# Optimization experiments

Hardware: AMD Instinct MI355X
Metric: run time of the kernel (lower is better)

The kernel has to match this reference:

```python
import jax, jax.numpy as jnp
import numpy as np

EPS = 1e-8


def setup_inputs() -> dict:
    key = jax.random.key(0)
    k1, k2, k3, k4, k5 = jax.random.split(key, 5)
    B, N_LOG, N_PHYS, E = 16, 512, 2048, 2048
    P = jax.random.uniform(k1, (B, N_LOG, N_PHYS), dtype=jnp.float32)
    d_hw = jax.random.randint(k2, (N_PHYS, N_PHYS), 0, 4, dtype=jnp.int32)
    edge_src = jax.random.randint(k3, (B, E), 0, N_LOG, dtype=jnp.int32)
    edge_dst = jax.random.randint(k4, (B, E), 0, N_LOG, dtype=jnp.int32)
    edge_w = jax.random.uniform(k5, (B, E), dtype=jnp.float32)
    return {"P": P, "d_hw": d_hw, "edge_src": edge_src,
            "edge_dst": edge_dst, "edge_w": edge_w}


def reference(P, d_hw, edge_src, edge_dst, edge_w):
    # A_hw[p,q] = 1 where hardware distance == 1 (adjacent qubits)
    A_hw = (d_hw == 1).astype(P.dtype)                      # [Q, Q]
    B = P.shape[0]
    # Dense contraction once per batch: PA[b,i,q] = sum_p P[b,i,p] A[p,q]
    PA = jnp.einsum('bip,pq->biq', P, A_hw)                 # [B, N, Q]
    b_idx = jnp.arange(B)[:, None]                          # [B, 1]
    gi = PA[b_idx, edge_src]                                # [B, E, Q]
    gj = P[b_idx, edge_dst]                                 # [B, E, Q]
    adj_score = jnp.einsum('beq,beq->be', gi, gj)           # [B, E]
    sample_adj = jnp.sum(edge_w * adj_score, axis=-1)       # [B]
    sample_weight = jnp.maximum(jnp.sum(edge_w, axis=-1), EPS)
    # every sample has edges -> valid_samples = B
    loss = -jnp.mean(sample_adj / sample_weight)
    return loss
```

## Files before the change

kernel.cpp:

```cpp
#include <hip/hip_runtime.h>
#include <hip/hip_bf16.h>

#define BATCH 16
#define NLOG 512
#define Q 2048
#define NEDGE 2048
#define M_TOT (BATCH * NLOG)
#define KB 2048

typedef float f32x4 __attribute__((ext_vector_type(4)));
typedef int i32x4 __attribute__((ext_vector_type(4)));
typedef int i32x8 __attribute__((ext_vector_type(8)));

__device__ __forceinline__ unsigned char to_e4m3(float f) {
    int pk = __builtin_amdgcn_cvt_pk_fp8_f32(f, f, 0, false);
    return (unsigned char)(pk & 0xff);
}

__global__ __launch_bounds__(256) void prep(const float* __restrict__ P,
                                            unsigned char* __restrict__ P8,
                                            const int* __restrict__ d_hw,
                                            unsigned char* __restrict__ A8t,
                                            float* __restrict__ adj,
                                            float* __restrict__ wsum,
                                            unsigned* __restrict__ counter) {
    int bid = blockIdx.x;
    if (bid == 0) {
        if (threadIdx.x == 0) *counter = 0u;
        if (threadIdx.x < BATCH) { adj[threadIdx.x] = 0.f; wsum[threadIdx.x] = 0.f; }
    }
    if (bid < 8192) {
        int i = (bid * 256 + threadIdx.x) * 8;
        float4 v0 = *(const float4*)(P + i);
        float4 v1 = *(const float4*)(P + i + 4);
        int lo = 0, hi = 0;
        lo = __builtin_amdgcn_cvt_pk_fp8_f32(v0.x, v0.y, lo, false);
        lo = __builtin_amdgcn_cvt_pk_fp8_f32(v0.z, v0.w, lo, true);
        hi = __builtin_amdgcn_cvt_pk_fp8_f32(v1.x, v1.y, hi, false);
        hi = __builtin_amdgcn_cvt_pk_fp8_f32(v1.z, v1.w, hi, true);
        int2 st; st.x = lo; st.y = hi;
        *(int2*)(P8 + i) = st;
    } else {
        bid -= 8192;
        __shared__ unsigned char tile[32][33];
        int q0 = (bid & 63) * 32;
        int p0 = (bid >> 6) * 32;
        int tx = threadIdx.x & 31;
        int ty = threadIdx.x >> 5;
        for (int s = 0; s < 32; s += 8) {
            int p = p0 + ty + s;
            int v = d_hw[(size_t)p * Q + q0 + tx];
            tile[ty + s][tx] = (v == 1) ? 0x38 : 0x00;
        }
        __syncthreads();
        for (int s = 0; s < 32; s += 8) {
            A8t[(size_t)(q0 + ty + s) * Q + p0 + tx] = tile[tx][ty + s];
        }
    }
}

__global__ __launch_bounds__(256, 2) void gemm_bt8(const unsigned char* __restrict__ A,
                                                   const unsigned char* __restrict__ Bt,
                                                   unsigned char* __restrict__ PA8) {
    __shared__ unsigned char As[32768];
    __shared__ unsigned char Bs[16384];

    const int t = threadIdx.x;
    const int w = t >> 6;
    const int wr = w >> 1, wc = w & 1;
    const int l = t & 63;
    const int quad = l >> 4;
    const int lane16 = l & 15;

    const int m0 = blockIdx.x * 256;
    const int n0 = blockIdx.y * 128;

    const int s_row = t >> 3;
    const int s_off = (((t & 7) ^ (s_row & 7)) << 4);

    const int r7 = lane16 & 7;
    const int c0 = ((2 * quad) ^ r7) << 4;
    const int c1 = ((2 * quad + 1) ^ r7) << 4;

    f32x4 acc[8][4] = {};

    for (int k0 = 0; k0 < KB; k0 += 128) {
        #pragma unroll
        for (int c = 0; c < 8; c++) {
            const unsigned char* g = A + (size_t)(m0 + c * 32 + s_row) * KB + k0 + s_off;
            __builtin_amdgcn_global_load_lds(
                (const __attribute__((address_space(1))) void*)g,
                (__attribute__((address_space(3))) void*)(As + c * 4096 + w * 1024),
                16, 0, 0);
        }
        #pragma unroll
        for (int c = 0; c < 4; c++) {
            const unsigned char* g = Bt + (size_t)(n0 + c * 32 + s_row) * KB + k0 + s_off;
            __builtin_amdgcn_global_load_lds(
                (const __attribute__((address_space(1))) void*)g,
                (__attribute__((address_space(3))) void*)(Bs + c * 4096 + w * 1024),
                16, 0, 0);
        }
        __syncthreads();

        i32x8 bfr[4];
        #pragma unroll
        for (int j = 0; j < 4; j++) {
            int base = (wc * 64 + j * 16 + lane16) << 7;
            i32x4 lo = *(const i32x4*)(Bs + base + c0);
            i32x4 hi = *(const i32x4*)(Bs + base + c1);
            bfr[j] = __builtin_shufflevector(lo, hi, 0, 1, 2, 3, 4, 5, 6, 7);
        }
        #pragma unroll
        for (int i = 0; i < 8; i++) {
            int base = (wr * 128 + i * 16 + lane16) << 7;
            i32x4 lo = *(const i32x4*)(As + base + c0);
            i32x4 hi = *(const i32x4*)(As + base + c1);
            i32x8 af = __builtin_shufflevector(lo, hi, 0, 1, 2, 3, 4, 5, 6, 7);
            #pragma unroll
            for (int j = 0; j < 4; j++)
                acc[i][j] = __builtin_amdgcn_mfma_scale_f32_16x16x128_f8f6f4(
                    af, bfr[j], acc[i][j], 0, 0,
                    0, 127,
                    0, 127);
        }
        __syncthreads();
    }

    #pragma unroll
    for (int i = 0; i < 8; i++) {
        #pragma unroll
        for (int j = 0; j < 4; j++) {
            #pragma unroll
            for (int r = 0; r < 4; r++) {
                int row = m0 + wr * 128 + i * 16 + quad * 4 + r;
                int col = n0 + wc * 64 + j * 16 + lane16;
                PA8[(size_t)row * Q + col] = to_e4m3(acc[i][j][r] * (1.0f / 256.0f));
            }
        }
    }
}

__global__ __launch_bounds__(256, 2) void edge_dot(const unsigned char* __restrict__ PA8,
                                                   const unsigned char* __restrict__ P8,
                                                   const int* __restrict__ esrc,
                                                   const int* __restrict__ edst,
                                                   const float* __restrict__ ew,
                                                   float* __restrict__ adj,
                                                   float* __restrict__ wsum,
                                                   unsigned* __restrict__ counter,
                                                   float* __restrict__ out) {
    const int lid = blockIdx.x;
    const int b   = (lid & 7) | ((lid >> 8) << 3);
    const int bx  = (lid >> 3) & 31;
    const int t = threadIdx.x;
    const int w = t >> 6;
    const int lane = t & 63;
    const int lane16 = lane & 15;
    const int quad = lane >> 4;

    const int eg = b * NEDGE + bx * 64 + w * 16 + lane16;
    const int src = esrc[eg];
    const int dst = edst[eg];
    const float we = ew[eg];

    const unsigned char* ap = PA8 + (size_t)(b * NLOG + src) * Q + quad * 32;
    const unsigned char* bp = P8  + (size_t)(b * NLOG + dst) * Q + quad * 32;

    f32x4 acc0 = {}, acc1 = {};
    #pragma unroll 2
    for (int k0 = 0; k0 < KB; k0 += 256) {
        i32x4 a0l = *(const i32x4*)(ap + k0);
        i32x4 a0h = *(const i32x4*)(ap + k0 + 16);
        i32x4 b0l = *(const i32x4*)(bp + k0);
        i32x4 b0h = *(const i32x4*)(bp + k0 + 16);
        i32x4 a1l = *(const i32x4*)(ap + k0 + 128);
        i32x4 a1h = *(const i32x4*)(ap + k0 + 144);
        i32x4 b1l = *(const i32x4*)(bp + k0 + 128);
        i32x4 b1h = *(const i32x4*)(bp + k0 + 144);
        acc0 = __builtin_amdgcn_mfma_scale_f32_16x16x128_f8f6f4(
            __builtin_shufflevector(a0l, a0h, 0, 1, 2, 3, 4, 5, 6, 7),
            __builtin_shufflevector(b0l, b0h, 0, 1, 2, 3, 4, 5, 6, 7),
            acc0, 0, 0, 0, 127, 0, 127);
        acc1 = __builtin_amdgcn_mfma_scale_f32_16x16x128_f8f6f4(
            __builtin_shufflevector(a1l, a1h, 0, 1, 2, 3, 4, 5, 6, 7),
            __builtin_shufflevector(b1l, b1h, 0, 1, 2, 3, 4, 5, 6, 7),
            acc1, 0, 0, 0, 127, 0, 127);
    }
    f32x4 accs = acc0 + acc1;

    const int r = lane16 & 3;
    float d = (r == 0) ? accs[0] : (r == 1) ? accs[1] : (r == 2) ? accs[2] : accs[3];
    float contrib = ((lane16 >> 2) == quad) ? we * d * 256.0f : 0.0f;
    float wpart = (quad == 0) ? we : 0.0f;
    #pragma unroll
    for (int off = 32; off > 0; off >>= 1) {
        contrib += __shfl_xor(contrib, off);
        wpart   += __shfl_xor(wpart, off);
    }

    __shared__ float ra[4], rw[4];
    if (lane == 0) { ra[w] = contrib; rw[w] = wpart; }
    __syncthreads();

    __shared__ unsigned done;
    if (t == 0) {
        atomicAdd(&adj[b],  ra[0] + ra[1] + ra[2] + ra[3]);
        atomicAdd(&wsum[b], rw[0] + rw[1] + rw[2] + rw[3]);
        __threadfence();
        done = atomicAdd(counter, 1u);
    }
    __syncthreads();
    if (t == 0 && done == 512 - 1) {
        __threadfence();
        float s = 0.f;
        #pragma unroll
        for (int bb = 0; bb < BATCH; bb++) {
            float av = atomicAdd(&adj[bb], 0.0f);
            float wv = atomicAdd(&wsum[bb], 0.0f);
            s += av / fmaxf(wv, 1e-8f);
        }
        out[0] = -s / (float)BATCH;
    }
}

extern "C" void kernel_launch(void* const* d_in, const int* in_sizes, int n_in,
                              void* d_out, int out_size, void* d_ws, size_t ws_size,
                              hipStream_t stream) {
    const float* P    = (const float*)d_in[0];
    const int* d_hw   = (const int*)d_in[1];
    const int* esrc   = (const int*)d_in[2];
    const int* edst   = (const int*)d_in[3];
    const float* ew   = (const float*)d_in[4];
    float* out        = (float*)d_out;

    char* ws = (char*)d_ws;
    unsigned char* P8  = (unsigned char*)ws;
    unsigned char* A8t = (unsigned char*)(ws + 16777216);
    unsigned char* PA8 = (unsigned char*)(ws + 20971520);
    float* adj         = (float*)(ws + 37748736);
    float* wsum        = (float*)(ws + 37748736 + 64);
    unsigned* counter  = (unsigned*)(ws + 37748736 + 128);

    prep<<<8192 + 4096, 256, 0, stream>>>(P, P8, d_hw, A8t, adj, wsum, counter);
    gemm_bt8<<<dim3(M_TOT / 256, Q / 128), 256, 0, stream>>>(P8, A8t, PA8);
    edge_dot<<<512, 256, 0, stream>>>(PA8, P8, esrc, edst, ew, adj, wsum, counter, out);
}
```

Baseline: 179.8 us.

## Split edge dot-product K dimension across warps and launch more edge_dot blocks

Each block now handles 16 edges rather than 64, and its four warps each cover a 512-element slice of the K dimension. Every warp issues all of its loads up front and then runs four MFMAs, instead of looping over the full 2048 elements. The grid grows from 512 to 2048 blocks and the launch-bounds occupancy hint rises to 8, aiming for more memory-level parallelism in this latency-bound gather. The cost is four times as many global atomics on adj, wsum and the counter.

```diff
diff --git a/kernel.cpp b/kernel.cpp
--- a/kernel.cpp
+++ b/kernel.cpp
@@ -7,6 +7,7 @@
 #define NEDGE 2048
 #define M_TOT (BATCH * NLOG)
 #define KB 2048
+#define EDOT_BLOCKS 2048
 
 typedef float f32x4 __attribute__((ext_vector_type(4)));
 typedef int i32x4 __attribute__((ext_vector_type(4)));
@@ -141,7 +142,7 @@
     }
 }
 
-__global__ __launch_bounds__(256, 2) void edge_dot(const unsigned char* __restrict__ PA8,
+__global__ __launch_bounds__(256, 8) void edge_dot(const unsigned char* __restrict__ PA8,
                                                    const unsigned char* __restrict__ P8,
                                                    const int* __restrict__ esrc,
                                                    const int* __restrict__ edst,
@@ -151,48 +152,55 @@
                                                    unsigned* __restrict__ counter,
                                                    float* __restrict__ out) {
     const int lid = blockIdx.x;
-    const int b   = (lid & 7) | ((lid >> 8) << 3);
-    const int bx  = (lid >> 3) & 31;
+    const int idx = lid >> 3;
+    const int b   = (lid & 7) | ((idx >> 7) << 3);
+    const int chunk = idx & 127;
     const int t = threadIdx.x;
     const int w = t >> 6;
     const int lane = t & 63;
     const int lane16 = lane & 15;
     const int quad = lane >> 4;
 
-    const int eg = b * NEDGE + bx * 64 + w * 16 + lane16;
+    const int eg = b * NEDGE + chunk * 16 + lane16;
     const int src = esrc[eg];
     const int dst = edst[eg];
     const float we = ew[eg];
 
-    const unsigned char* ap = PA8 + (size_t)(b * NLOG + src) * Q + quad * 32;
-    const unsigned char* bp = P8  + (size_t)(b * NLOG + dst) * Q + quad * 32;
+    const unsigned char* ap = PA8 + (size_t)(b * NLOG + src) * Q + w * 512 + quad * 32;
+    const unsigned char* bp = P8  + (size_t)(b * NLOG + dst) * Q + w * 512 + quad * 32;
+
+    i32x4 al[4][2], bl[4][2];
+    #pragma unroll
+    for (int c = 0; c < 4; c++) {
+        al[c][0] = *(const i32x4*)(ap + c * 128);
+        al[c][1] = *(const i32x4*)(ap + c * 128 + 16);
+        bl[c][0] = *(const i32x4*)(bp + c * 128);
+        bl[c][1] = *(const i32x4*)(bp + c * 128 + 16);
+    }
 
     f32x4 acc0 = {}, acc1 = {};
-    #pragma unroll 2
-    for (int k0 = 0; k0 < KB; k0 += 256) {
-        i32x4 a0l = *(const i32x4*)(ap + k0);
-        i32x4 a0h = *(const i32x4*)(ap + k0 + 16);
-        i32x4 b0l = *(const i32x4*)(bp + k0);
-        i32x4 b0h = *(const i32x4*)(bp + k0 + 16);
-        i32x4 a1l = *(const i32x4*)(ap + k0 + 128);
-        i32x4 a1h = *(const i32x4*)(ap + k0 + 144);
-        i32x4 b1l = *(const i32x4*)(bp + k0 + 128);
-        i32x4 b1h = *(const i32x4*)(bp + k0 + 144);
-        acc0 = __builtin_amdgcn_mfma_scale_f32_16x16x128_f8f6f4(
-            __builtin_shufflevector(a0l, a0h, 0, 1, 2, 3, 4, 5, 6, 7),
-            __builtin_shufflevector(b0l, b0h, 0, 1, 2, 3, 4, 5, 6, 7),
-            acc0, 0, 0, 0, 127, 0, 127);
-        acc1 = __builtin_amdgcn_mfma_scale_f32_16x16x128_f8f6f4(
-            __builtin_shufflevector(a1l, a1h, 0, 1, 2, 3, 4, 5, 6, 7),
-            __builtin_shufflevector(b1l, b1h, 0, 1, 2, 3, 4, 5, 6, 7),
-            acc1, 0, 0, 0, 127, 0, 127);
-    }
+    acc0 = __builtin_amdgcn_mfma_scale_f32_16x16x128_f8f6f4(
+        __builtin_shufflevector(al[0][0], al[0][1], 0, 1, 2, 3, 4, 5, 6, 7),
+        __builtin_shufflevector(bl[0][0], bl[0][1], 0, 1, 2, 3, 4, 5, 6, 7),
+        acc0, 0, 0, 0, 127, 0, 127);
+    acc1 = __builtin_amdgcn_mfma_scale_f32_16x16x128_f8f6f4(
+        __builtin_shufflevector(al[1][0], al[1][1], 0, 1, 2, 3, 4, 5, 6, 7),
+        __builtin_shufflevector(bl[1][0], bl[1][1], 0, 1, 2, 3, 4, 5, 6, 7),
+        acc1, 0, 0, 0, 127, 0, 127);
+    acc0 = __builtin_amdgcn_mfma_scale_f32_16x16x128_f8f6f4(
+        __builtin_shufflevector(al[2][0], al[2][1], 0, 1, 2, 3, 4, 5, 6, 7),
+        __builtin_shufflevector(bl[2][0], bl[2][1], 0, 1, 2, 3, 4, 5, 6, 7),
+        acc0, 0, 0, 0, 127, 0, 127);
+    acc1 = __builtin_amdgcn_mfma_scale_f32_16x16x128_f8f6f4(
+        __builtin_shufflevector(al[3][0], al[3][1], 0, 1, 2, 3, 4, 5, 6, 7),
+        __builtin_shufflevector(bl[3][0], bl[3][1], 0, 1, 2, 3, 4, 5, 6, 7),
+        acc1, 0, 0, 0, 127, 0, 127);
     f32x4 accs = acc0 + acc1;
 
     const int r = lane16 & 3;
     float d = (r == 0) ? accs[0] : (r == 1) ? accs[1] : (r == 2) ? accs[2] : accs[3];
     float contrib = ((lane16 >> 2) == quad) ? we * d * 256.0f : 0.0f;
-    float wpart = (quad == 0) ? we : 0.0f;
+    float wpart = (w == 0 && quad == 0) ? we : 0.0f;
     #pragma unroll
     for (int off = 32; off > 0; off >>= 1) {
         contrib += __shfl_xor(contrib, off);
@@ -211,7 +219,7 @@
         done = atomicAdd(counter, 1u);
     }
     __syncthreads();
-    if (t == 0 && done == 512 - 1) {
+    if (t == 0 && done == EDOT_BLOCKS - 1) {
         __threadfence();
         float s = 0.f;
         #pragma unroll
@@ -244,5 +252,5 @@
 
     prep<<<8192 + 4096, 256, 0, stream>>>(P, P8, d_hw, A8t, adj, wsum, counter);
     gemm_bt8<<<dim3(M_TOT / 256, Q / 128), 256, 0, stream>>>(P8, A8t, PA8);
-    edge_dot<<<512, 256, 0, stream>>>(PA8, P8, esrc, edst, ew, adj, wsum, counter, out);
-}
+    edge_dot<<<EDOT_BLOCKS, 256, 0, stream>>>(PA8, P8, esrc, edst, ew, adj, wsum, counter, out);
+}
```

After: 218.0 us. +21.2%, slower.

## Rewrite edge_dot as wave-per-edge scalar fp8 dots with prefetching

Applied to the files above, without the earlier changes.

The edge dot-product kernel no longer uses MFMA, where only the diagonal of each 16x16 tile was useful. Each wavefront now walks 16 edges, with each lane converting and dotting a 32-byte slice of the two fp8 rows in scalar FP32. The next edge's rows are prefetched in software while the current one is computed. Blocks grow to 512 threads, half as many are launched, and the finishing reduction is folded into a single thread. The aim is to stop wasting matrix-core work and to get better memory-level parallelism on the gathered rows, at the cost of many more conversion and FMA ALU instructions.

```diff
diff --git a/kernel.cpp b/kernel.cpp
--- a/kernel.cpp
+++ b/kernel.cpp
@@ -7,7 +7,9 @@
 #define NEDGE 2048
 #define M_TOT (BATCH * NLOG)
 #define KB 2048
-
+#define EDOT_BLOCKS 256
+
+typedef float f32x2 __attribute__((ext_vector_type(2)));
 typedef float f32x4 __attribute__((ext_vector_type(4)));
 typedef int i32x4 __attribute__((ext_vector_type(4)));
 typedef int i32x8 __attribute__((ext_vector_type(8)));
@@ -15,6 +17,20 @@
 __device__ __forceinline__ unsigned char to_e4m3(float f) {
     int pk = __builtin_amdgcn_cvt_pk_fp8_f32(f, f, 0, false);
     return (unsigned char)(pk & 0xff);
+}
+
+__device__ __forceinline__ float dot16(i32x4 a, i32x4 b) {
+    float s0 = 0.f, s1 = 0.f;
+    #pragma unroll
+    for (int d = 0; d < 4; d++) {
+        f32x2 alo = __builtin_amdgcn_cvt_pk_f32_fp8(a[d], false);
+        f32x2 ahi = __builtin_amdgcn_cvt_pk_f32_fp8(a[d], true);
+        f32x2 blo = __builtin_amdgcn_cvt_pk_f32_fp8(b[d], false);
+        f32x2 bhi = __builtin_amdgcn_cvt_pk_f32_fp8(b[d], true);
+        s0 += alo[0] * blo[0] + alo[1] * blo[1];
+        s1 += ahi[0] * bhi[0] + ahi[1] * bhi[1];
+    }
+    return s0 + s1;
 }
 
 __global__ __launch_bounds__(256) void prep(const float* __restrict__ P,
@@ -141,86 +157,83 @@
     }
 }
 
-__global__ __launch_bounds__(256, 2) void edge_dot(const unsigned char* __restrict__ PA8,
-                                                   const unsigned char* __restrict__ P8,
-                                                   const int* __restrict__ esrc,
-                                                   const int* __restrict__ edst,
-                                                   const float* __restrict__ ew,
-                                                   float* __restrict__ adj,
-                                                   float* __restrict__ wsum,
-                                                   unsigned* __restrict__ counter,
-                                                   float* __restrict__ out) {
+__global__ __launch_bounds__(512) void edge_dot(const unsigned char* __restrict__ PA8,
+                                                const unsigned char* __restrict__ P8,
+                                                const int* __restrict__ esrc,
+                                                const int* __restrict__ edst,
+                                                const float* __restrict__ ew,
+                                                float* __restrict__ adj,
+                                                float* __restrict__ wsum,
+                                                unsigned* __restrict__ counter,
+                                                float* __restrict__ out) {
     const int lid = blockIdx.x;
-    const int b   = (lid & 7) | ((lid >> 8) << 3);
-    const int bx  = (lid >> 3) & 31;
+    const int b = (lid & 7) | ((lid >> 7) << 3);
+    const int chunk = (lid >> 3) & 15;
     const int t = threadIdx.x;
     const int w = t >> 6;
     const int lane = t & 63;
-    const int lane16 = lane & 15;
-    const int quad = lane >> 4;
-
-    const int eg = b * NEDGE + bx * 64 + w * 16 + lane16;
-    const int src = esrc[eg];
-    const int dst = edst[eg];
-    const float we = ew[eg];
-
-    const unsigned char* ap = PA8 + (size_t)(b * NLOG + src) * Q + quad * 32;
-    const unsigned char* bp = P8  + (size_t)(b * NLOG + dst) * Q + quad * 32;
-
-    f32x4 acc0 = {}, acc1 = {};
-    #pragma unroll 2
-    for (int k0 = 0; k0 < KB; k0 += 256) {
-        i32x4 a0l = *(const i32x4*)(ap + k0);
-        i32x4 a0h = *(const i32x4*)(ap + k0 + 16);
-        i32x4 b0l = *(const i32x4*)(bp + k0);
-        i32x4 b0h = *(const i32x4*)(bp + k0 + 16);
-        i32x4 a1l = *(const i32x4*)(ap + k0 + 128);
-        i32x4 a1h = *(const i32x4*)(ap + k0 + 144);
-        i32x4 b1l = *(const i32x4*)(bp + k0 + 128);
-        i32x4 b1h = *(const i32x4*)(bp + k0 + 144);
-        acc0 = __builtin_amdgcn_mfma_scale_f32_16x16x128_f8f6f4(
-            __builtin_shufflevector(a0l, a0h, 0, 1, 2, 3, 4, 5, 6, 7),
-            __builtin_shufflevector(b0l, b0h, 0, 1, 2, 3, 4, 5, 6, 7),
-            acc0, 0, 0, 0, 127, 0, 127);
-        acc1 = __builtin_amdgcn_mfma_scale_f32_16x16x128_f8f6f4(
-            __builtin_shufflevector(a1l, a1h, 0, 1, 2, 3, 4, 5, 6, 7),
-            __builtin_shufflevector(b1l, b1h, 0, 1, 2, 3, 4, 5, 6, 7),
-            acc1, 0, 0, 0, 127, 0, 127);
-    }
-    f32x4 accs = acc0 + acc1;
-
-    const int r = lane16 & 3;
-    float d = (r == 0) ? accs[0] : (r == 1) ? accs[1] : (r == 2) ? accs[2] : accs[3];
-    float contrib = ((lane16 >> 2) == quad) ? we * d * 256.0f : 0.0f;
-    float wpart = (quad == 0) ? we : 0.0f;
-    #pragma unroll
-    for (int off = 32; off > 0; off >>= 1) {
-        contrib += __shfl_xor(contrib, off);
-        wpart   += __shfl_xor(wpart, off);
-    }
-
-    __shared__ float ra[4], rw[4];
-    if (lane == 0) { ra[w] = contrib; rw[w] = wpart; }
+
+    const int e0 = b * NEDGE + chunk * 128 + w * 16;
+    const unsigned char* Ab = PA8 + (size_t)b * NLOG * Q;
+    const unsigned char* Bb = P8  + (size_t)b * NLOG * Q;
+    const int off = lane * 32;
+
+    int src = esrc[e0], dst = edst[e0];
+    float wcur = ew[e0];
+    const unsigned char* ap = Ab + (size_t)src * Q + off;
+    const unsigned char* bp = Bb + (size_t)dst * Q + off;
+    i32x4 A0 = *(const i32x4*)ap;
+    i32x4 A1 = *(const i32x4*)(ap + 16);
+    i32x4 B0 = *(const i32x4*)bp;
+    i32x4 B1 = *(const i32x4*)(bp + 16);
+
+    float acc = 0.f;
+    float wacc = 0.f;
+    #pragma unroll
+    for (int e = 0; e < 16; e++) {
+        i32x4 nA0 = A0, nA1 = A1, nB0 = B0, nB1 = B1;
+        float wnext = 0.f;
+        if (e < 15) {
+            int ns = esrc[e0 + e + 1], nd = edst[e0 + e + 1];
+            wnext = ew[e0 + e + 1];
+            const unsigned char* nap = Ab + (size_t)ns * Q + off;
+            const unsigned char* nbp = Bb + (size_t)nd * Q + off;
+            nA0 = *(const i32x4*)nap;
+            nA1 = *(const i32x4*)(nap + 16);
+            nB0 = *(const i32x4*)nbp;
+            nB1 = *(const i32x4*)(nbp + 16);
+        }
+        float p = dot16(A0, B0) + dot16(A1, B1);
+        acc += wcur * p;
+        wacc += wcur;
+        A0 = nA0; A1 = nA1; B0 = nB0; B1 = nB1; wcur = wnext;
+    }
+
+    #pragma unroll
+    for (int o = 32; o > 0; o >>= 1) acc += __shfl_xor(acc, o);
+
+    __shared__ float ra[8], rw[8];
+    if (lane == 0) { ra[w] = acc; rw[w] = wacc; }
     __syncthreads();
 
-    __shared__ unsigned done;
     if (t == 0) {
-        atomicAdd(&adj[b],  ra[0] + ra[1] + ra[2] + ra[3]);
-        atomicAdd(&wsum[b], rw[0] + rw[1] + rw[2] + rw[3]);
+        float a = 0.f, ws = 0.f;
+        #pragma unroll
+        for (int i = 0; i < 8; i++) { a += ra[i]; ws += rw[i]; }
+        atomicAdd(&adj[b],  a * 256.0f);
+        atomicAdd(&wsum[b], ws);
         __threadfence();
-        done = atomicAdd(counter, 1u);
-    }
-    __syncthreads();
-    if (t == 0 && done == 512 - 1) {
-        __threadfence();
-        float s = 0.f;
-        #pragma unroll
-        for (int bb = 0; bb < BATCH; bb++) {
-            float av = atomicAdd(&adj[bb], 0.0f);
-            float wv = atomicAdd(&wsum[bb], 0.0f);
-            s += av / fmaxf(wv, 1e-8f);
-        }
-        out[0] = -s / (float)BATCH;
+        if (atomicAdd(counter, 1u) == EDOT_BLOCKS - 1) {
+            __threadfence();
+            float s = 0.f;
+            #pragma unroll
+            for (int bb = 0; bb < BATCH; bb++) {
+                float av = atomicAdd(&adj[bb], 0.0f);
+                float wv = atomicAdd(&wsum[bb], 0.0f);
+                s += av / fmaxf(wv, 1e-8f);
+            }
+            out[0] = -s / (float)BATCH;
+        }
     }
 }
 
@@ -244,5 +257,5 @@
 
     prep<<<8192 + 4096, 256, 0, stream>>>(P, P8, d_hw, A8t, adj, wsum, counter);
     gemm_bt8<<<dim3(M_TOT / 256, Q / 128), 256, 0, stream>>>(P8, A8t, PA8);
-    edge_dot<<<512, 256, 0, stream>>>(PA8, P8, esrc, edst, ew, adj, wsum, counter, out);
-}
+    edge_dot<<<EDOT_BLOCKS, 512, 0, stream>>>(PA8, P8, esrc, edst, ew, adj, wsum, counter, out);
+}
```

New measurement: 167.5 us. 1.07x faster.

## Replace edge gather-dot with dense edge-weight matrix GEMM and pipelined fp8 GEMMs

Applied to the files above, without the earlier changes.

Rather than gathering rows per edge, this builds a dense per-batch edge-weight matrix W[dst,src] with atomics, quantizes it to fp8, and computes the loss as a second GEMM (W times PA) reduced elementwise against P. The first GEMM now writes PA transposed. Both GEMMs use 512-thread blocks with double-buffered LDS, interleaved global-to-LDS staging, and priority hints. This removes random per-edge row gathers, but adds extra kernels, a 16MB fp32 W buffer to zero and quantize, and fp8 rounding of the accumulated edge weights (scaled by 0.25), which can lose precision.

```diff
diff --git a/kernel.cpp b/kernel.cpp
--- a/kernel.cpp
+++ b/kernel.cpp
@@ -7,7 +7,9 @@
 #define NEDGE 2048
 #define M_TOT (BATCH * NLOG)
 #define KB 2048
-
+#define GEMMB_BLOCKS 256
+
+typedef float f32x2 __attribute__((ext_vector_type(2)));
 typedef float f32x4 __attribute__((ext_vector_type(4)));
 typedef int i32x4 __attribute__((ext_vector_type(4)));
 typedef int i32x8 __attribute__((ext_vector_type(8)));
@@ -15,12 +17,17 @@
 __device__ __forceinline__ unsigned char to_e4m3(float f) {
     int pk = __builtin_amdgcn_cvt_pk_fp8_f32(f, f, 0, false);
     return (unsigned char)(pk & 0xff);
+}
+__device__ __forceinline__ float fp8_to_f32(unsigned char v) {
+    f32x2 p = __builtin_amdgcn_cvt_pk_f32_fp8((int)v, false);
+    return p[0];
 }
 
 __global__ __launch_bounds__(256) void prep(const float* __restrict__ P,
                                             unsigned char* __restrict__ P8,
                                             const int* __restrict__ d_hw,
                                             unsigned char* __restrict__ A8t,
+                                            float* __restrict__ W32,
                                             float* __restrict__ adj,
                                             float* __restrict__ wsum,
                                             unsigned* __restrict__ counter) {
@@ -40,7 +47,7 @@
         hi = __builtin_amdgcn_cvt_pk_fp8_f32(v1.z, v1.w, hi, true);
         int2 st; st.x = lo; st.y = hi;
         *(int2*)(P8 + i) = st;
-    } else {
+    } else if (bid < 12288) {
         bid -= 8192;
         __shared__ unsigned char tile[32][33];
         int q0 = (bid & 63) * 32;
@@ -56,76 +63,164 @@
         for (int s = 0; s < 32; s += 8) {
             A8t[(size_t)(q0 + ty + s) * Q + p0 + tx] = tile[tx][ty + s];
         }
-    }
-}
-
-__global__ __launch_bounds__(256, 2) void gemm_bt8(const unsigned char* __restrict__ A,
-                                                   const unsigned char* __restrict__ Bt,
-                                                   unsigned char* __restrict__ PA8) {
-    __shared__ unsigned char As[32768];
-    __shared__ unsigned char Bs[16384];
-
+    } else {
+        size_t off = ((size_t)(bid - 12288) * 256 + threadIdx.x) * 16;
+        int4 z = {0, 0, 0, 0};
+        *(int4*)((char*)W32 + off) = z;
+    }
+}
+
+__global__ __launch_bounds__(256) void w_build(const int* __restrict__ esrc,
+                                               const int* __restrict__ edst,
+                                               const float* __restrict__ ew,
+                                               float* __restrict__ W32,
+                                               float* __restrict__ wsum) {
+    const int b = blockIdx.x;
     const int t = threadIdx.x;
-    const int w = t >> 6;
-    const int wr = w >> 1, wc = w & 1;
-    const int l = t & 63;
-    const int quad = l >> 4;
-    const int lane16 = l & 15;
-
+    float wacc = 0.f;
+    #pragma unroll
+    for (int k = 0; k < NEDGE / 256; k++) {
+        int e = b * NEDGE + k * 256 + t;
+        int src = esrc[e];
+        int dst = edst[e];
+        float we = ew[e];
+        atomicAdd(W32 + (size_t)b * NLOG * NLOG + dst * NLOG + src, we);
+        wacc += we;
+    }
+    #pragma unroll
+    for (int o = 32; o > 0; o >>= 1) wacc += __shfl_xor(wacc, o);
+    __shared__ float rw[4];
+    if ((t & 63) == 0) rw[t >> 6] = wacc;
+    __syncthreads();
+    if (t == 0) wsum[b] = rw[0] + rw[1] + rw[2] + rw[3];
+}
+
+__global__ __launch_bounds__(256) void wquant(const float* __restrict__ W32,
+                                              unsigned char* __restrict__ W8t) {
+    int i = (blockIdx.x * 256 + threadIdx.x) * 8;
+    float4 v0 = *(const float4*)(W32 + i);
+    float4 v1 = *(const float4*)(W32 + i + 4);
+    int lo = 0, hi = 0;
+    lo = __builtin_amdgcn_cvt_pk_fp8_f32(v0.x * 0.25f, v0.y * 0.25f, lo, false);
+    lo = __builtin_amdgcn_cvt_pk_fp8_f32(v0.z * 0.25f, v0.w * 0.25f, lo, true);
+    hi = __builtin_amdgcn_cvt_pk_fp8_f32(v1.x * 0.25f, v1.y * 0.25f, hi, false);
+    hi = __builtin_amdgcn_cvt_pk_fp8_f32(v1.z * 0.25f, v1.w * 0.25f, hi, true);
+    int2 st; st.x = lo; st.y = hi;
+    *(int2*)(W8t + i) = st;
+}
+
+#define MF(af, bf, accv) __builtin_amdgcn_mfma_scale_f32_16x16x128_f8f6f4( \
+    (af), (bf), (accv), 0, 0, 0, 127, 0, 127)
+
+#define READ_FRAG(buf, rowbase) __extension__({                                \
+    const int _b = ((rowbase) + lane16) << 7;                                  \
+    i32x4 _lo = *(const i32x4*)((buf) + _b + c0);                              \
+    i32x4 _hi = *(const i32x4*)((buf) + _b + c1);                              \
+    __builtin_shufflevector(_lo, _hi, 0, 1, 2, 3, 4, 5, 6, 7); })
+
+#define STAGE(srcp, stride, rowoff, dstbuf, c, kk0)                            \
+    __builtin_amdgcn_global_load_lds(                                          \
+        (const __attribute__((address_space(1))) void*)((srcp) +               \
+            (size_t)((rowoff) + (c) * 64 + s_row) * (stride) + (kk0) + s_off), \
+        (__attribute__((address_space(3))) void*)((dstbuf) + (c) * 8192 + t * 16), \
+        16, 0, 0)
+
+#define KTILE_BODY(as, bs, DO_STAGE_A, DO_STAGE_B)                             \
+    {                                                                          \
+        i32x8 bf0 = READ_FRAG(bs, wc * 64 + 0);                                \
+        i32x8 bf1 = READ_FRAG(bs, wc * 64 + 16);                               \
+        i32x8 bf2 = READ_FRAG(bs, wc * 64 + 32);                               \
+        i32x8 bf3 = READ_FRAG(bs, wc * 64 + 48);                               \
+        i32x8 af0 = READ_FRAG(as, wr * 128 + 0);                               \
+        i32x8 af1 = READ_FRAG(as, wr * 128 + 16);                              \
+        if (st) { DO_STAGE_A(0); DO_STAGE_A(1); DO_STAGE_A(2); }               \
+        __builtin_amdgcn_s_barrier();                                          \
+        __builtin_amdgcn_s_setprio(1);                                         \
+        acc[0][0] = MF(af0, bf0, acc[0][0]); acc[0][1] = MF(af0, bf1, acc[0][1]); \
+        acc[0][2] = MF(af0, bf2, acc[0][2]); acc[0][3] = MF(af0, bf3, acc[0][3]); \
+        acc[1][0] = MF(af1, bf0, acc[1][0]); acc[1][1] = MF(af1, bf1, acc[1][1]); \
+        acc[1][2] = MF(af1, bf2, acc[1][2]); acc[1][3] = MF(af1, bf3, acc[1][3]); \
+        __builtin_amdgcn_s_setprio(0);                                         \
+        __builtin_amdgcn_s_barrier();                                          \
+        i32x8 af2 = READ_FRAG(as, wr * 128 + 32);                              \
+        i32x8 af3 = READ_FRAG(as, wr * 128 + 48);                              \
+        if (st) { DO_STAGE_A(3); DO_STAGE_B(0); DO_STAGE_B(1); }               \
+        __builtin_amdgcn_s_barrier();                                          \
+        __builtin_amdgcn_s_setprio(1);                                         \
+        acc[2][0] = MF(af2, bf0, acc[2][0]); acc[2][1] = MF(af2, bf1, acc[2][1]); \
+        acc[2][2] = MF(af2, bf2, acc[2][2]); acc[2][3] = MF(af2, bf3, acc[2][3]); \
+        acc[3][0] = MF(af3, bf0, acc[3][0]); acc[3][1] = MF(af3, bf1, acc[3][1]); \
+        acc[3][2] = MF(af3, bf2, acc[3][2]); acc[3][3] = MF(af3, bf3, acc[3][3]); \
+        __builtin_amdgcn_s_setprio(0);                                         \
+        __builtin_amdgcn_s_barrier();                                          \
+        i32x8 af4 = READ_FRAG(as, wr * 128 + 64);                              \
+        i32x8 af5 = READ_FRAG(as, wr * 128 + 80);                              \
+        if (st) { DO_STAGE_B(2); DO_STAGE_B(3); }                              \
+        __builtin_amdgcn_s_barrier();                                          \
+        __builtin_amdgcn_s_setprio(1);                                         \
+        acc[4][0] = MF(af4, bf0, acc[4][0]); acc[4][1] = MF(af4, bf1, acc[4][1]); \
+        acc[4][2] = MF(af4, bf2, acc[4][2]); acc[4][3] = MF(af4, bf3, acc[4][3]); \
+        acc[5][0] = MF(af5, bf0, acc[5][0]); acc[5][1] = MF(af5, bf1, acc[5][1]); \
+        acc[5][2] = MF(af5, bf2, acc[5][2]); acc[5][3] = MF(af5, bf3, acc[5][3]); \
+        __builtin_amdgcn_s_setprio(0);                                         \
+        __builtin_amdgcn_s_barrier();                                          \
+        i32x8 af6 = READ_FRAG(as, wr * 128 + 96);                              \
+        i32x8 af7 = READ_FRAG(as, wr * 128 + 112);                             \
+        __builtin_amdgcn_s_barrier();                                          \
+        __builtin_amdgcn_s_setprio(1);                                         \
+        acc[6][0] = MF(af6, bf0, acc[6][0]); acc[6][1] = MF(af6, bf1, acc[6][1]); \
+        acc[6][2] = MF(af6, bf2, acc[6][2]); acc[6][3] = MF(af6, bf3, acc[6][3]); \
+        acc[7][0] = MF(af7, bf0, acc[7][0]); acc[7][1] = MF(af7, bf1, acc[7][1]); \
+        acc[7][2] = MF(af7, bf2, acc[7][2]); acc[7][3] = MF(af7, bf3, acc[7][3]); \
+        __builtin_amdgcn_s_setprio(0);                                         \
+        asm volatile("s_waitcnt vmcnt(0)" ::: "memory");                       \
+        __builtin_amdgcn_s_barrier();                                          \
+    }
+
+#define GEMM_COMMON_DECLS                                                      \
+    const int t = threadIdx.x;                                                 \
+    const int w = t >> 6;                                                      \
+    const int wr = w >> 2, wc = w & 3;                                         \
+    const int l = t & 63;                                                      \
+    const int quad = l >> 4;                                                   \
+    const int lane16 = l & 15;                                                 \
+    const int s_row = t >> 3;                                                  \
+    const int s_off = (((t & 7) ^ (s_row & 7)) << 4);                          \
+    const int r7 = lane16 & 7;                                                 \
+    const int c0 = ((2 * quad) ^ r7) << 4;                                     \
+    const int c1 = ((2 * quad + 1) ^ r7) << 4;
+
+__global__ __launch_bounds__(512, 2) void gemm_a(const unsigned char* __restrict__ At,
+                                                 const unsigned char* __restrict__ Pp,
+                                                 unsigned char* __restrict__ PA8t) {
+    __shared__ unsigned char As[2][32768];
+    __shared__ unsigned char Bs[2][32768];
+    GEMM_COMMON_DECLS
     const int m0 = blockIdx.x * 256;
-    const int n0 = blockIdx.y * 128;
-
-    const int s_row = t >> 3;
-    const int s_off = (((t & 7) ^ (s_row & 7)) << 4);
-
-    const int r7 = lane16 & 7;
-    const int c0 = ((2 * quad) ^ r7) << 4;
-    const int c1 = ((2 * quad + 1) ^ r7) << 4;
+    const int n0 = blockIdx.y * 256;
 
     f32x4 acc[8][4] = {};
 
-    for (int k0 = 0; k0 < KB; k0 += 128) {
-        #pragma unroll
-        for (int c = 0; c < 8; c++) {
-            const unsigned char* g = A + (size_t)(m0 + c * 32 + s_row) * KB + k0 + s_off;
-            __builtin_amdgcn_global_load_lds(
-                (const __attribute__((address_space(1))) void*)g,
-                (__attribute__((address_space(3))) void*)(As + c * 4096 + w * 1024),
-                16, 0, 0);
-        }
-        #pragma unroll
-        for (int c = 0; c < 4; c++) {
-            const unsigned char* g = Bt + (size_t)(n0 + c * 32 + s_row) * KB + k0 + s_off;
-            __builtin_amdgcn_global_load_lds(
-                (const __attribute__((address_space(1))) void*)g,
-                (__attribute__((address_space(3))) void*)(Bs + c * 4096 + w * 1024),
-                16, 0, 0);
-        }
-        __syncthreads();
-
-        i32x8 bfr[4];
-        #pragma unroll
-        for (int j = 0; j < 4; j++) {
-            int base = (wc * 64 + j * 16 + lane16) << 7;
-            i32x4 lo = *(const i32x4*)(Bs + base + c0);
-            i32x4 hi = *(const i32x4*)(Bs + base + c1);
-            bfr[j] = __builtin_shufflevector(lo, hi, 0, 1, 2, 3, 4, 5, 6, 7);
-        }
-        #pragma unroll
-        for (int i = 0; i < 8; i++) {
-            int base = (wr * 128 + i * 16 + lane16) << 7;
-            i32x4 lo = *(const i32x4*)(As + base + c0);
-            i32x4 hi = *(const i32x4*)(As + base + c1);
-            i32x8 af = __builtin_shufflevector(lo, hi, 0, 1, 2, 3, 4, 5, 6, 7);
-            #pragma unroll
-            for (int j = 0; j < 4; j++)
-                acc[i][j] = __builtin_amdgcn_mfma_scale_f32_16x16x128_f8f6f4(
-                    af, bfr[j], acc[i][j], 0, 0,
-                    0, 127,
-                    0, 127);
-        }
-        __syncthreads();
-    }
+#define SA_A(c) STAGE(At, Q, m0, an, c, kn)
+#define SB_A(c) STAGE(Pp, Q, n0, bn, c, kn)
+    {
+        unsigned char* an = As[0]; unsigned char* bn = Bs[0];
+        const int kn = 0;
+        SA_A(0); SA_A(1); SA_A(2); SA_A(3);
+        SB_A(0); SB_A(1); SB_A(2); SB_A(3);
+    }
+    __syncthreads();
+    for (int kt = 0; kt < 16; ++kt) {
+        const unsigned char* as = As[kt & 1];
+        const unsigned char* bs = Bs[kt & 1];
+        unsigned char* an = As[(kt + 1) & 1];
+        unsigned char* bn = Bs[(kt + 1) & 1];
+        const int kn = (kt + 1) * 128;
+        const bool st = (kt < 15);
+        KTILE_BODY(as, bs, SA_A, SB_A)
+    }
+#undef SA_A
+#undef SB_A
 
     #pragma unroll
     for (int i = 0; i < 8; i++) {
@@ -135,92 +230,86 @@
             for (int r = 0; r < 4; r++) {
                 int row = m0 + wr * 128 + i * 16 + quad * 4 + r;
                 int col = n0 + wc * 64 + j * 16 + lane16;
-                PA8[(size_t)row * Q + col] = to_e4m3(acc[i][j][r] * (1.0f / 256.0f));
+                PA8t[(size_t)row * M_TOT + col] = to_e4m3(acc[i][j][r] * (1.0f / 256.0f));
             }
         }
     }
 }
 
-__global__ __launch_bounds__(256, 2) void edge_dot(const unsigned char* __restrict__ PA8,
-                                                   const unsigned char* __restrict__ P8,
-                                                   const int* __restrict__ esrc,
-                                                   const int* __restrict__ edst,
-                                                   const float* __restrict__ ew,
-                                                   float* __restrict__ adj,
-                                                   float* __restrict__ wsum,
-                                                   unsigned* __restrict__ counter,
-                                                   float* __restrict__ out) {
-    const int lid = blockIdx.x;
-    const int b   = (lid & 7) | ((lid >> 8) << 3);
-    const int bx  = (lid >> 3) & 31;
-    const int t = threadIdx.x;
-    const int w = t >> 6;
-    const int lane = t & 63;
-    const int lane16 = lane & 15;
-    const int quad = lane >> 4;
-
-    const int eg = b * NEDGE + bx * 64 + w * 16 + lane16;
-    const int src = esrc[eg];
-    const int dst = edst[eg];
-    const float we = ew[eg];
-
-    const unsigned char* ap = PA8 + (size_t)(b * NLOG + src) * Q + quad * 32;
-    const unsigned char* bp = P8  + (size_t)(b * NLOG + dst) * Q + quad * 32;
-
-    f32x4 acc0 = {}, acc1 = {};
-    #pragma unroll 2
-    for (int k0 = 0; k0 < KB; k0 += 256) {
-        i32x4 a0l = *(const i32x4*)(ap + k0);
-        i32x4 a0h = *(const i32x4*)(ap + k0 + 16);
-        i32x4 b0l = *(const i32x4*)(bp + k0);
-        i32x4 b0h = *(const i32x4*)(bp + k0 + 16);
-        i32x4 a1l = *(const i32x4*)(ap + k0 + 128);
-        i32x4 a1h = *(const i32x4*)(ap + k0 + 144);
-        i32x4 b1l = *(const i32x4*)(bp + k0 + 128);
-        i32x4 b1h = *(const i32x4*)(bp + k0 + 144);
-        acc0 = __builtin_amdgcn_mfma_scale_f32_16x16x128_f8f6f4(
-            __builtin_shufflevector(a0l, a0h, 0, 1, 2, 3, 4, 5, 6, 7),
-            __builtin_shufflevector(b0l, b0h, 0, 1, 2, 3, 4, 5, 6, 7),
-            acc0, 0, 0, 0, 127, 0, 127);
-        acc1 = __builtin_amdgcn_mfma_scale_f32_16x16x128_f8f6f4(
-            __builtin_shufflevector(a1l, a1h, 0, 1, 2, 3, 4, 5, 6, 7),
-            __builtin_shufflevector(b1l, b1h, 0, 1, 2, 3, 4, 5, 6, 7),
-            acc1, 0, 0, 0, 127, 0, 127);
-    }
-    f32x4 accs = acc0 + acc1;
-
-    const int r = lane16 & 3;
-    float d = (r == 0) ? accs[0] : (r == 1) ? accs[1] : (r == 2) ? accs[2] : accs[3];
-    float contrib = ((lane16 >> 2) == quad) ? we * d * 256.0f : 0.0f;
-    float wpart = (quad == 0) ? we : 0.0f;
-    #pragma unroll
-    for (int off = 32; off > 0; off >>= 1) {
-        contrib += __shfl_xor(contrib, off);
-        wpart   += __shfl_xor(wpart, off);
-    }
-
-    __shared__ float ra[4], rw[4];
-    if (lane == 0) { ra[w] = contrib; rw[w] = wpart; }
+__global__ __launch_bounds__(512, 2) void gemm_b(const unsigned char* __restrict__ Wt,
+                                                 const unsigned char* __restrict__ PAt,
+                                                 const unsigned char* __restrict__ Pp,
+                                                 float* __restrict__ adj,
+                                                 const float* __restrict__ wsum,
+                                                 unsigned* __restrict__ counter,
+                                                 float* __restrict__ out) {
+    __shared__ unsigned char As[2][32768];
+    __shared__ unsigned char Bs[2][32768];
+    __shared__ float rs[8];
+    GEMM_COMMON_DECLS
+    const int m0 = blockIdx.x * 256;
+    const int n0 = blockIdx.y * 256;
+    const int b = blockIdx.x >> 1;
+    const int kbase = b * NLOG;
+
+    f32x4 acc[8][4] = {};
+
+#define SA_B(c) STAGE(Wt, NLOG, m0, an, c, kn)
+#define SB_B(c) STAGE(PAt + kbase, M_TOT, n0, bn, c, kn)
+    {
+        unsigned char* an = As[0]; unsigned char* bn = Bs[0];
+        const int kn = 0;
+        SA_B(0); SA_B(1); SA_B(2); SA_B(3);
+        SB_B(0); SB_B(1); SB_B(2); SB_B(3);
+    }
     __syncthreads();
-
-    __shared__ unsigned done;
+    for (int kt = 0; kt < 4; ++kt) {
+        const unsigned char* as = As[kt & 1];
+        const unsigned char* bs = Bs[kt & 1];
+        unsigned char* an = As[(kt + 1) & 1];
+        unsigned char* bn = Bs[(kt + 1) & 1];
+        const int kn = (kt + 1) * 128;
+        const bool st = (kt < 3);
+        KTILE_BODY(as, bs, SA_B, SB_B)
+    }
+#undef SA_B
+#undef SB_B
+
+    float s = 0.f;
+    #pragma unroll
+    for (int i = 0; i < 8; i++) {
+        #pragma unroll
+        for (int j = 0; j < 4; j++) {
+            #pragma unroll
+            for (int r = 0; r < 4; r++) {
+                int row = m0 + wr * 128 + i * 16 + quad * 4 + r;
+                int col = n0 + wc * 64 + j * 16 + lane16;
+                s += acc[i][j][r] * fp8_to_f32(Pp[(size_t)row * Q + col]);
+            }
+        }
+    }
+    #pragma unroll
+    for (int o = 32; o > 0; o >>= 1) s += __shfl_xor(s, o);
+    if (l == 0) rs[w] = s;
+    __syncthreads();
+
     if (t == 0) {
-        atomicAdd(&adj[b],  ra[0] + ra[1] + ra[2] + ra[3]);
-        atomicAdd(&wsum[b], rw[0] + rw[1] + rw[2] + rw[3]);
+        float a = 0.f;
+        #pragma unroll
+        for (int i = 0; i < 8; i++) a += rs[i];
+        atomicAdd(&adj[b], a * 1024.0f);
         __threadfence();
-        done = atomicAdd(counter, 1u);
-    }
-    __syncthreads();
-    if (t == 0 && done == 512 - 1) {
-        __threadfence();
-        float s = 0.f;
-        #pragma unroll
-        for (int bb = 0; bb < BATCH; bb++) {
-            float av = atomicAdd(&adj[bb], 0.0f);
-            float wv = atomicAdd(&wsum[bb], 0.0f);
-            s += av / fmaxf(wv, 1e-8f);
-        }
-        out[0] = -s / (float)BATCH;
+        if (atomicAdd(counter, 1u) == GEMMB_BLOCKS - 1) {
+            __threadfence();
+            float sm = 0.f;
+            #pragma unroll
+            for (int bb = 0; bb < BATCH; bb++) {
+                float av = atomicAdd(&adj[bb], 0.0f);
+                float wv = atomicAdd((float*)&wsum[bb], 0.0f);
+                sm += av / fmaxf(wv, 1e-8f);
+            }
+            out[0] = -sm / (float)BATCH;
+        }
     }
 }
 
@@ -235,14 +324,18 @@
     float* out        = (float*)d_out;
 
     char* ws = (char*)d_ws;
-    unsigned char* P8  = (unsigned char*)ws;
-    unsigned char* A8t = (unsigned char*)(ws + 16777216);
-    unsigned char* PA8 = (unsigned char*)(ws + 20971520);
-    float* adj         = (float*)(ws + 37748736);
-    float* wsum        = (float*)(ws + 37748736 + 64);
-    unsigned* counter  = (unsigned*)(ws + 37748736 + 128);
-
-    prep<<<8192 + 4096, 256, 0, stream>>>(P, P8, d_hw, A8t, adj, wsum, counter);
-    gemm_bt8<<<dim3(M_TOT / 256, Q / 128), 256, 0, stream>>>(P8, A8t, PA8);
-    edge_dot<<<512, 256, 0, stream>>>(PA8, P8, esrc, edst, ew, adj, wsum, counter, out);
-}
+    unsigned char* P8   = (unsigned char*)ws;
+    unsigned char* A8t  = (unsigned char*)(ws + 16777216);
+    unsigned char* PA8t = (unsigned char*)(ws + 20971520);
+    float* W32          = (float*)(ws + 37748736);
+    unsigned char* W8t  = (unsigned char*)(ws + 54525952);
+    float* adj          = (float*)(ws + 58720256);
+    float* wsum         = (float*)(ws + 58720256 + 64);
+    unsigned* counter   = (unsigned*)(ws + 58720256 + 128);
+
+    prep<<<16384, 256, 0, stream>>>(P, P8, d_hw, A8t, W32, adj, wsum, counter);
+    w_build<<<BATCH, 256, 0, stream>>>(esrc, edst, ew, W32, wsum);
+    wquant<<<2048, 256, 0, stream>>>(W32, W8t);
+    gemm_a<<<dim3(Q / 256, M_TOT / 256), 512, 0, stream>>>(A8t, P8, PA8t);
+    gemm_b<<<dim3(M_TOT / 256, Q / 256), 512, 0, stream>>>(W8t, PA8t, P8, adj, wsum, counter, out);
+}
```

New measurement: 193.9 us. 1.08x slower.
